# Kernel tuning notes

Measured on AMD Instinct MI355X. Metric: run time of the kernel, lower is better.

Reference implementation:

```python
import jax, jax.numpy as jnp
import numpy as np

B, S, D, H, O = 4, 128, 768, 768, 2

def setup_inputs() -> dict:
    key = jax.random.key(0)
    ks = jax.random.split(key, 6)
    scale = 1.0 / np.sqrt(2 * D)
    return {
        "a": jax.random.normal(ks[0], (B, S, D), jnp.float32),
        "b": jax.random.normal(ks[1], (B, S, D), jnp.float32),
        "W1": jax.random.normal(ks[2], (2 * D, H), jnp.float32) * scale,
        "b1": jax.random.normal(ks[3], (H,), jnp.float32) * 0.01,
        "W2": jax.random.normal(ks[4], (H, O), jnp.float32) * (1.0 / np.sqrt(H)),
        "b2": jax.random.normal(ks[5], (O,), jnp.float32) * 0.01,
    }

def reference(a, b, W1, b1, W2, b2):
    # Pairwise concat [a_i ; b_j] followed by Linear(2D->H) is algebraically
    # identical to projecting a and b separately and broadcast-adding
    # (biaffine-style rewrite; same math as cat+matmul, less HBM traffic).
    d = a.shape[-1]
    ha = jnp.einsum('bsd,dh->bsh', a, W1[:d])        # (B, Sa, H)
    hb = jnp.einsum('btd,dh->bth', b, W1[d:])        # (B, Sb, H)
    h = jax.nn.relu(ha[:, :, None, :] + hb[:, None, :, :] + b1)  # (B, Sa, Sb, H)
    scores = jnp.einsum('bsth,ho->bsto', h, W2) + b2  # (B, Sa, Sb, O)
    return scores
```

## Files before the change

kernel.cpp:

```cpp
#include <hip/hip_runtime.h>
#include <hip/hip_fp16.h>


typedef __attribute__((ext_vector_type(2))) _Float16 half2t;
typedef __attribute__((ext_vector_type(8))) _Float16 half8t;
typedef __attribute__((ext_vector_type(4))) float floatx4;
typedef unsigned int uint;

__device__ __forceinline__ half2t pkrtz(float x, float y) {
    __fp16 r __attribute__((ext_vector_type(2))) = __builtin_amdgcn_cvt_pkrtz(x, y);
    half2t o; __builtin_memcpy(&o, &r, 4); return o;
}

__global__ __launch_bounds__(256) void gemm_kernel(
    const float* __restrict__ a, const float* __restrict__ bmat,
    const float* __restrict__ W1, const float* __restrict__ b1,
    const float* __restrict__ W2,
    ushort* __restrict__ Hf,
    uint* __restrict__ W2pk)
{
    const int which = blockIdx.z;
    const int n0 = blockIdx.x * 32;
    const int m0 = blockIdx.y * 32;
    const int t  = threadIdx.x;

    if (blockIdx.x == 0 && blockIdx.y == 0 && which == 0) {
#pragma unroll
        for (int j = t; j < 768; j += 256) {
            const int o  = (j >= 384) ? 1 : 0;
            const int h2 = j - o * 384;
            half2t pw = pkrtz(W2[4 * h2 + o], W2[4 * h2 + 2 + o]);
            uint u; __builtin_memcpy(&u, &pw, 4);
            W2pk[j] = u;
        }
    }

    __shared__ ushort As[2][32][72];
    __shared__ ushort Bs[2][32][72];

    const int arow = t >> 3;
    const int akc  = (t & 7) * 8;
    const float* __restrict__ Asrc = which ? bmat : a;
    const float* __restrict__ aptr = Asrc + (size_t)(m0 + arow) * 768 + akc;

    const int ncol = t & 31;
    const int kg   = (t >> 5) * 8;
    const float* __restrict__ bptr = W1 + (size_t)(which * 768 + kg) * 768 + n0 + ncol;

    const int lane = t & 63;
    const int w    = t >> 6;
    const int mh   = w >> 1;
    const int nh   = w & 1;
    const int lr   = lane & 15;
    const int lq   = lane >> 4;

    floatx4 acc = {0, 0, 0, 0};

    float4 a4[2];
    float  br[8];
    a4[0] = *(const float4*)(aptr);
    a4[1] = *(const float4*)(aptr + 4);
#pragma unroll
    for (int j = 0; j < 8; j++) br[j] = bptr[(size_t)j * 768];

    int p = 0;
    for (int kt = 0; kt < 768; kt += 64, p ^= 1) {
        float4 a4n[2];
        float  brn[8];
        if (kt + 64 < 768) {
            a4n[0] = *(const float4*)(aptr + kt + 64);
            a4n[1] = *(const float4*)(aptr + kt + 68);
#pragma unroll
            for (int j = 0; j < 8; j++)
                brn[j] = bptr[(size_t)(kt + 64 + j) * 768];
        }

        half2t ap[4];
        ap[0] = pkrtz(a4[0].x, a4[0].y);
        ap[1] = pkrtz(a4[0].z, a4[0].w);
        ap[2] = pkrtz(a4[1].x, a4[1].y);
        ap[3] = pkrtz(a4[1].z, a4[1].w);
        __builtin_memcpy(&As[p][arow][akc], ap, 16);
        half2t bp[4];
#pragma unroll
        for (int j = 0; j < 4; j++) bp[j] = pkrtz(br[2 * j], br[2 * j + 1]);
        __builtin_memcpy(&Bs[p][ncol][kg], bp, 16);

        __syncthreads();

#pragma unroll
        for (int h = 0; h < 2; h++) {
            const int kb = h * 32 + lq * 8;
            half8t afr, bfr;
            __builtin_memcpy(&afr, &As[p][mh * 16 + lr][kb], 16);
            __builtin_memcpy(&bfr, &Bs[p][nh * 16 + lr][kb], 16);
            acc = __builtin_amdgcn_mfma_f32_16x16x32_f16(afr, bfr, acc, 0, 0, 0);
        }

        a4[0] = a4n[0]; a4[1] = a4n[1];
#pragma unroll
        for (int j = 0; j < 8; j++) br[j] = brn[j];
    }

    const int ncolO = n0 + nh * 16 + lr;
    const float bias = which ? 0.f : b1[ncolO];
    ushort* __restrict__ dst = Hf + (size_t)which * 393216 + ncolO;
    const int rbase = m0 + mh * 16 + lq * 4;
#pragma unroll
    for (int r = 0; r < 4; r++) {
        _Float16 v = (_Float16)(acc[r] + bias);
        ushort u; __builtin_memcpy(&u, &v, 2);
        dst[(size_t)(rbase + r) * 768] = u;
    }
}

__global__ __launch_bounds__(256) void pair_kernel(
    const ushort* __restrict__ Hf, const uint* __restrict__ W2pk,
    const float* __restrict__ b2, float* __restrict__ out)
{
    const int bb = blockIdx.z >> 2;
    const int hh = blockIdx.z & 3;
    const int s0 = blockIdx.y * 16;
    const int t0 = blockIdx.x * 16;
    const int tid = threadIdx.x;

    __shared__ ushort hAs[16][200];
    __shared__ ushort hBs[16][200];

    const int hbase = hh * 192;
    const ushort* __restrict__ Asrc = Hf +          (size_t)(bb * 128 + s0) * 768 + hbase;
    const ushort* __restrict__ Bsrc = Hf + 393216 + (size_t)(bb * 128 + t0) * 768 + hbase;

#pragma unroll
    for (int i = 0; i < 3; i++) {
        const int c   = tid + i * 256;
        const int arr = c >= 384;
        const int cc  = c - arr * 384;
        const int row = cc / 24;
        const int ch  = (cc % 24) * 8;
        const ushort* src = arr ? Bsrc : Asrc;
        ushort* dst = arr ? &hBs[row][ch] : &hAs[row][ch];
        *(uint4*)dst = *(const uint4*)(src + (size_t)row * 768 + ch);
    }
    __syncthreads();

    const int sl = tid >> 4;
    const int tl = tid & 15;
    const ushort* __restrict__ arow = &hAs[sl][0];
    const ushort* __restrict__ brow = &hBs[tl][0];
    const uint* __restrict__ w2o0 = W2pk +       hh * 96;
    const uint* __restrict__ w2o1 = W2pk + 384 + hh * 96;

    float acc0 = 0.f, acc1 = 0.f;
    const half2t zero = {(_Float16)0.f, (_Float16)0.f};

#pragma unroll 8
    for (int h8 = 0; h8 < 192; h8 += 8) {
        half2t pa[4], pb[4], w0[4], w1[4];
        __builtin_memcpy(pa, arow + h8, 16);
        __builtin_memcpy(pb, brow + h8, 16);
        __builtin_memcpy(w0, &w2o0[h8 / 2], 16);
        __builtin_memcpy(w1, &w2o1[h8 / 2], 16);
#pragma unroll
        for (int j = 0; j < 4; j++) {
            half2t s = pa[j] + pb[j];
            s = __builtin_elementwise_max(s, zero);
            acc0 = __builtin_amdgcn_fdot2(s, w0[j], acc0, false);
            acc1 = __builtin_amdgcn_fdot2(s, w1[j], acc1, false);
        }
    }

    if (hh == 0) { acc0 += b2[0]; acc1 += b2[1]; }
    const int sg = bb * 128 + s0 + sl;
    const int tg = t0 + tl;
    float* ob = &out[((size_t)sg * 128 + tg) * 2];
    unsafeAtomicAdd(ob,     acc0);
    unsafeAtomicAdd(ob + 1, acc1);
}

extern "C" void kernel_launch(void* const* d_in, const int* in_sizes, int n_in,
                              void* d_out, int out_size, void* d_ws, size_t ws_size,
                              hipStream_t stream) {
    const float* a  = (const float*)d_in[0];
    const float* b  = (const float*)d_in[1];
    const float* W1 = (const float*)d_in[2];
    const float* b1 = (const float*)d_in[3];
    const float* W2 = (const float*)d_in[4];
    const float* b2 = (const float*)d_in[5];
    float* out = (float*)d_out;

    ushort* Hf   = (ushort*)d_ws;
    uint*   W2pk = (uint*)((char*)d_ws + (2 << 20));

    gemm_kernel<<<dim3(24, 16, 2), 256, 0, stream>>>(a, b, W1, b1, W2, Hf, W2pk);
    pair_kernel<<<dim3(8, 8, 16), 256, 0, stream>>>(Hf, W2pk, b2, out);
}
```

Measured before the change: 83.10 us.

## Load GEMM A fragments directly to registers; widen pair tile to 32 columns

In the GEMM kernel, each lane now loads its MFMA A-operand fp32 values straight from global memory and converts them in registers, dropping the As shared-memory staging buffer. Rows are duplicated across the two nh waves, so global A traffic rises while LDS writes and reads fall. The pair kernel now handles 32 t-columns per block, so each thread computes two outputs. This reuses the A row and W2 loads, halves the grid, and adds registers and more LDS for hBs.

```diff
diff --git a/kernel.cpp b/kernel.cpp
--- a/kernel.cpp
+++ b/kernel.cpp
@@ -35,13 +35,7 @@
         }
     }
 
-    __shared__ ushort As[2][32][72];
     __shared__ ushort Bs[2][32][72];
-
-    const int arow = t >> 3;
-    const int akc  = (t & 7) * 8;
-    const float* __restrict__ Asrc = which ? bmat : a;
-    const float* __restrict__ aptr = Asrc + (size_t)(m0 + arow) * 768 + akc;
 
     const int ncol = t & 31;
     const int kg   = (t >> 5) * 8;
@@ -54,33 +48,35 @@
     const int lr   = lane & 15;
     const int lq   = lane >> 4;
 
+    const float* __restrict__ Asrc = which ? bmat : a;
+    const float* __restrict__ afp =
+        Asrc + (size_t)(m0 + mh * 16 + lr) * 768 + lq * 8;
+
     floatx4 acc = {0, 0, 0, 0};
 
-    float4 a4[2];
+    float4 af[4];
     float  br[8];
-    a4[0] = *(const float4*)(aptr);
-    a4[1] = *(const float4*)(aptr + 4);
+    af[0] = *(const float4*)(afp);
+    af[1] = *(const float4*)(afp + 4);
+    af[2] = *(const float4*)(afp + 32);
+    af[3] = *(const float4*)(afp + 36);
 #pragma unroll
     for (int j = 0; j < 8; j++) br[j] = bptr[(size_t)j * 768];
 
     int p = 0;
     for (int kt = 0; kt < 768; kt += 64, p ^= 1) {
-        float4 a4n[2];
+        float4 afn[4];
         float  brn[8];
         if (kt + 64 < 768) {
-            a4n[0] = *(const float4*)(aptr + kt + 64);
-            a4n[1] = *(const float4*)(aptr + kt + 68);
+            afn[0] = *(const float4*)(afp + kt + 64);
+            afn[1] = *(const float4*)(afp + kt + 68);
+            afn[2] = *(const float4*)(afp + kt + 96);
+            afn[3] = *(const float4*)(afp + kt + 100);
 #pragma unroll
             for (int j = 0; j < 8; j++)
                 brn[j] = bptr[(size_t)(kt + 64 + j) * 768];
         }
 
-        half2t ap[4];
-        ap[0] = pkrtz(a4[0].x, a4[0].y);
-        ap[1] = pkrtz(a4[0].z, a4[0].w);
-        ap[2] = pkrtz(a4[1].x, a4[1].y);
-        ap[3] = pkrtz(a4[1].z, a4[1].w);
-        __builtin_memcpy(&As[p][arow][akc], ap, 16);
         half2t bp[4];
 #pragma unroll
         for (int j = 0; j < 4; j++) bp[j] = pkrtz(br[2 * j], br[2 * j + 1]);
@@ -90,14 +86,21 @@
 
 #pragma unroll
         for (int h = 0; h < 2; h++) {
+            half2t ah[4];
+            ah[0] = pkrtz(af[2 * h].x, af[2 * h].y);
+            ah[1] = pkrtz(af[2 * h].z, af[2 * h].w);
+            ah[2] = pkrtz(af[2 * h + 1].x, af[2 * h + 1].y);
+            ah[3] = pkrtz(af[2 * h + 1].z, af[2 * h + 1].w);
+            half8t afr; __builtin_memcpy(&afr, ah, 16);
+
             const int kb = h * 32 + lq * 8;
-            half8t afr, bfr;
-            __builtin_memcpy(&afr, &As[p][mh * 16 + lr][kb], 16);
+            half8t bfr;
             __builtin_memcpy(&bfr, &Bs[p][nh * 16 + lr][kb], 16);
             acc = __builtin_amdgcn_mfma_f32_16x16x32_f16(afr, bfr, acc, 0, 0, 0);
         }
 
-        a4[0] = a4n[0]; a4[1] = a4n[1];
+#pragma unroll
+        for (int j = 0; j < 4; j++) af[j] = afn[j];
 #pragma unroll
         for (int j = 0; j < 8; j++) br[j] = brn[j];
     }
@@ -121,18 +124,18 @@
     const int bb = blockIdx.z >> 2;
     const int hh = blockIdx.z & 3;
     const int s0 = blockIdx.y * 16;
-    const int t0 = blockIdx.x * 16;
+    const int t0 = blockIdx.x * 32;
     const int tid = threadIdx.x;
 
     __shared__ ushort hAs[16][200];
-    __shared__ ushort hBs[16][200];
+    __shared__ ushort hBs[32][200];
 
     const int hbase = hh * 192;
     const ushort* __restrict__ Asrc = Hf +          (size_t)(bb * 128 + s0) * 768 + hbase;
     const ushort* __restrict__ Bsrc = Hf + 393216 + (size_t)(bb * 128 + t0) * 768 + hbase;
 
 #pragma unroll
-    for (int i = 0; i < 3; i++) {
+    for (int i = 0; i < 4; i++) {
         const int c   = tid + i * 256;
         const int arr = c >= 384;
         const int cc  = c - arr * 384;
@@ -142,40 +145,57 @@
         ushort* dst = arr ? &hBs[row][ch] : &hAs[row][ch];
         *(uint4*)dst = *(const uint4*)(src + (size_t)row * 768 + ch);
     }
+    if (tid < 128) {
+        const int cc  = 640 + tid;
+        const int row = cc / 24;
+        const int ch  = (cc % 24) * 8;
+        *(uint4*)&hBs[row][ch] = *(const uint4*)(Bsrc + (size_t)row * 768 + ch);
+    }
     __syncthreads();
 
     const int sl = tid >> 4;
     const int tl = tid & 15;
-    const ushort* __restrict__ arow = &hAs[sl][0];
-    const ushort* __restrict__ brow = &hBs[tl][0];
+    const ushort* __restrict__ arow  = &hAs[sl][0];
+    const ushort* __restrict__ brow0 = &hBs[tl][0];
+    const ushort* __restrict__ brow1 = &hBs[tl + 16][0];
     const uint* __restrict__ w2o0 = W2pk +       hh * 96;
     const uint* __restrict__ w2o1 = W2pk + 384 + hh * 96;
 
-    float acc0 = 0.f, acc1 = 0.f;
+    float a00 = 0.f, a01 = 0.f, a10 = 0.f, a11 = 0.f;
     const half2t zero = {(_Float16)0.f, (_Float16)0.f};
 
-#pragma unroll 8
+#pragma unroll 4
     for (int h8 = 0; h8 < 192; h8 += 8) {
-        half2t pa[4], pb[4], w0[4], w1[4];
-        __builtin_memcpy(pa, arow + h8, 16);
-        __builtin_memcpy(pb, brow + h8, 16);
+        half2t pa[4], pb0[4], pb1[4], w0[4], w1[4];
+        __builtin_memcpy(pa,  arow  + h8, 16);
+        __builtin_memcpy(pb0, brow0 + h8, 16);
+        __builtin_memcpy(pb1, brow1 + h8, 16);
         __builtin_memcpy(w0, &w2o0[h8 / 2], 16);
         __builtin_memcpy(w1, &w2o1[h8 / 2], 16);
 #pragma unroll
         for (int j = 0; j < 4; j++) {
-            half2t s = pa[j] + pb[j];
-            s = __builtin_elementwise_max(s, zero);
-            acc0 = __builtin_amdgcn_fdot2(s, w0[j], acc0, false);
-            acc1 = __builtin_amdgcn_fdot2(s, w1[j], acc1, false);
-        }
-    }
-
-    if (hh == 0) { acc0 += b2[0]; acc1 += b2[1]; }
+            half2t s0v = pa[j] + pb0[j];
+            half2t s1v = pa[j] + pb1[j];
+            s0v = __builtin_elementwise_max(s0v, zero);
+            s1v = __builtin_elementwise_max(s1v, zero);
+            a00 = __builtin_amdgcn_fdot2(s0v, w0[j], a00, false);
+            a01 = __builtin_amdgcn_fdot2(s0v, w1[j], a01, false);
+            a10 = __builtin_amdgcn_fdot2(s1v, w0[j], a10, false);
+            a11 = __builtin_amdgcn_fdot2(s1v, w1[j], a11, false);
+        }
+    }
+
+    if (hh == 0) {
+        const float c0 = b2[0], c1 = b2[1];
+        a00 += c0; a01 += c1; a10 += c0; a11 += c1;
+    }
     const int sg = bb * 128 + s0 + sl;
-    const int tg = t0 + tl;
-    float* ob = &out[((size_t)sg * 128 + tg) * 2];
-    unsafeAtomicAdd(ob,     acc0);
-    unsafeAtomicAdd(ob + 1, acc1);
+    float* ob0 = &out[((size_t)sg * 128 + t0 + tl) * 2];
+    float* ob1 = &out[((size_t)sg * 128 + t0 + tl + 16) * 2];
+    unsafeAtomicAdd(ob0,     a00);
+    unsafeAtomicAdd(ob0 + 1, a01);
+    unsafeAtomicAdd(ob1,     a10);
+    unsafeAtomicAdd(ob1 + 1, a11);
 }
 
 extern "C" void kernel_launch(void* const* d_in, const int* in_sizes, int n_in,
@@ -193,5 +213,5 @@
     uint*   W2pk = (uint*)((char*)d_ws + (2 << 20));
 
     gemm_kernel<<<dim3(24, 16, 2), 256, 0, stream>>>(a, b, W1, b1, W2, Hf, W2pk);
-    pair_kernel<<<dim3(8, 8, 16), 256, 0, stream>>>(Hf, W2pk, b2, out);
-}
+    pair_kernel<<<dim3(4, 8, 16), 256, 0, stream>>>(Hf, W2pk, b2, out);
+}
```

Result: slower. 95.90 us (+15.4%).

## Fuse GEMM and pair kernels into one cooperative launch with grid sync

Applied to the files above, without the earlier changes.

Merges the projection GEMM and the pairwise relu-dot kernel into a single cooperative kernel of 1024 blocks. Blocks first do GEMM tiles (or pack W2), then synchronise across the whole grid, then each runs one pair tile. This removes the second kernel launch and its gap, at the cost of a grid-wide barrier and a combined shared-memory footprint that may lower occupancy. If the cooperative launch fails it falls back to the two-kernel path.

```diff
diff --git a/kernel.cpp b/kernel.cpp
--- a/kernel.cpp
+++ b/kernel.cpp
@@ -1,5 +1,8 @@
 #include <hip/hip_runtime.h>
 #include <hip/hip_fp16.h>
+#include <hip/hip_cooperative_groups.h>
+
+namespace cg = cooperative_groups;
 
 
 typedef __attribute__((ext_vector_type(2))) _Float16 half2t;
@@ -12,28 +15,26 @@
     half2t o; __builtin_memcpy(&o, &r, 4); return o;
 }
 
-__global__ __launch_bounds__(256) void gemm_kernel(
+__device__ __forceinline__ void w2pack_body(const float* __restrict__ W2,
+                                            uint* __restrict__ W2pk) {
+    const int t = threadIdx.x;
+#pragma unroll
+    for (int j = t; j < 768; j += 256) {
+        const int o  = (j >= 384) ? 1 : 0;
+        const int h2 = j - o * 384;
+        half2t pw = pkrtz(W2[4 * h2 + o], W2[4 * h2 + 2 + o]);
+        uint u; __builtin_memcpy(&u, &pw, 4);
+        W2pk[j] = u;
+    }
+}
+
+__device__ __forceinline__ void gemm_body(
+    int n0, int m0, int which,
     const float* __restrict__ a, const float* __restrict__ bmat,
     const float* __restrict__ W1, const float* __restrict__ b1,
-    const float* __restrict__ W2,
-    ushort* __restrict__ Hf,
-    uint* __restrict__ W2pk)
-{
-    const int which = blockIdx.z;
-    const int n0 = blockIdx.x * 32;
-    const int m0 = blockIdx.y * 32;
-    const int t  = threadIdx.x;
-
-    if (blockIdx.x == 0 && blockIdx.y == 0 && which == 0) {
-#pragma unroll
-        for (int j = t; j < 768; j += 256) {
-            const int o  = (j >= 384) ? 1 : 0;
-            const int h2 = j - o * 384;
-            half2t pw = pkrtz(W2[4 * h2 + o], W2[4 * h2 + 2 + o]);
-            uint u; __builtin_memcpy(&u, &pw, 4);
-            W2pk[j] = u;
-        }
-    }
+    ushort* __restrict__ Hf)
+{
+    const int t = threadIdx.x;
 
     __shared__ ushort As[2][32][72];
     __shared__ ushort Bs[2][32][72];
@@ -114,14 +115,11 @@
     }
 }
 
-__global__ __launch_bounds__(256) void pair_kernel(
+__device__ __forceinline__ void pair_body(
+    int t0, int s0, int bb, int hh,
     const ushort* __restrict__ Hf, const uint* __restrict__ W2pk,
     const float* __restrict__ b2, float* __restrict__ out)
 {
-    const int bb = blockIdx.z >> 2;
-    const int hh = blockIdx.z & 3;
-    const int s0 = blockIdx.y * 16;
-    const int t0 = blockIdx.x * 16;
     const int tid = threadIdx.x;
 
     __shared__ ushort hAs[16][200];
@@ -176,6 +174,50 @@
     float* ob = &out[((size_t)sg * 128 + tg) * 2];
     unsafeAtomicAdd(ob,     acc0);
     unsafeAtomicAdd(ob + 1, acc1);
+}
+
+__global__ __launch_bounds__(256, 4) void fused_kernel(
+    const float* __restrict__ a, const float* __restrict__ bmat,
+    const float* __restrict__ W1, const float* __restrict__ b1,
+    const float* __restrict__ W2, const float* __restrict__ b2,
+    ushort* __restrict__ Hf, uint* __restrict__ W2pk,
+    float* __restrict__ out)
+{
+    const int bid = blockIdx.x;
+
+    if (bid < 768) {
+        const int which = bid >= 384;
+        const int rem   = bid - which * 384;
+        gemm_body((rem % 24) * 32, (rem / 24) * 32, which, a, bmat, W1, b1, Hf);
+    } else if (bid == 768) {
+        w2pack_body(W2, W2pk);
+    }
+
+    cg::this_grid().sync();
+
+    const int x = bid & 7;
+    const int y = (bid >> 3) & 7;
+    const int z = bid >> 6;
+    pair_body(x * 16, y * 16, z >> 2, z & 3, Hf, W2pk, b2, out);
+}
+
+__global__ __launch_bounds__(256) void gemm_kernel(
+    const float* __restrict__ a, const float* __restrict__ bmat,
+    const float* __restrict__ W1, const float* __restrict__ b1,
+    const float* __restrict__ W2,
+    ushort* __restrict__ Hf, uint* __restrict__ W2pk)
+{
+    if (blockIdx.x == 0 && blockIdx.y == 0 && blockIdx.z == 0)
+        w2pack_body(W2, W2pk);
+    gemm_body(blockIdx.x * 32, blockIdx.y * 32, blockIdx.z, a, bmat, W1, b1, Hf);
+}
+
+__global__ __launch_bounds__(256) void pair_kernel(
+    const ushort* __restrict__ Hf, const uint* __restrict__ W2pk,
+    const float* __restrict__ b2, float* __restrict__ out)
+{
+    pair_body(blockIdx.x * 16, blockIdx.y * 16, blockIdx.z >> 2, blockIdx.z & 3,
+              Hf, W2pk, b2, out);
 }
 
 extern "C" void kernel_launch(void* const* d_in, const int* in_sizes, int n_in,
@@ -192,6 +234,13 @@
     ushort* Hf   = (ushort*)d_ws;
     uint*   W2pk = (uint*)((char*)d_ws + (2 << 20));
 
-    gemm_kernel<<<dim3(24, 16, 2), 256, 0, stream>>>(a, b, W1, b1, W2, Hf, W2pk);
-    pair_kernel<<<dim3(8, 8, 16), 256, 0, stream>>>(Hf, W2pk, b2, out);
-}
+    void* args[] = {(void*)&a, (void*)&b, (void*)&W1, (void*)&b1, (void*)&W2,
+                    (void*)&b2, (void*)&Hf, (void*)&W2pk, (void*)&out};
+    hipError_t e = hipLaunchCooperativeKernel((const void*)fused_kernel,
+                                              dim3(1024), dim3(256),
+                                              args, 0, stream);
+    if (e != hipSuccess) {
+        gemm_kernel<<<dim3(24, 16, 2), 256, 0, stream>>>(a, b, W1, b1, W2, Hf, W2pk);
+        pair_kernel<<<dim3(8, 8, 16), 256, 0, stream>>>(Hf, W2pk, b2, out);
+    }
+}
```

Measured after the change: 240.2 us. +189.0%, slower.
